# Performance work log

Hardware: AMD Instinct MI355X
Metric: run time of the kernel (lower is better)

The kernel has to match this reference:

```python
import jax, jax.numpy as jnp
import numpy as np
import math

BN_EPS = 1e-5
BASES = [5, 4]
NH = 8    # num_heads
KD = 64   # key_dim = hidden_dim

def _bn(x, g, b, m, v):
    # eval-mode BatchNorm1d over channel dim of (B, C, L)
    s = g * jax.lax.rsqrt(v + BN_EPS)
    return (x - m[None, :, None]) * s[None, :, None] + b[None, :, None]

def _conv1x1(x, W):
    # W: (out_ch, in_ch), x: (B, C, L)
    return jnp.einsum('oc,bcl->bol', W, x)

def _dwconv3(x, W):
    # depthwise conv1d, kernel 3, pad 1. W: (C, 3)
    c = x.shape[1]
    return jax.lax.conv_general_dilated(
        x, W[:, None, :], window_strides=(1,), padding=((1, 1),),
        dimension_numbers=('NCH', 'OIH', 'NCH'), feature_group_count=c)

def _log_attn(x, base, qkW, qkg, qkb, qkm, qkv, vW, vg, vb, vm, vv,
              peW, peg, peb, pem, pev):
    b, c, w = x.shape
    hd = c // NH
    scale = KD ** -0.5
    n = int(math.log(w, base) - 1e-9) + 1
    L = base ** n
    xp = jnp.pad(x, ((0, 0), (0, 0), (0, L - w)))
    qk = _bn(_conv1x1(xp, qkW), qkg, qkb, qkm, qkv).reshape(b, NH, 2, KD, L)
    q, k = qk[:, :, 0], qk[:, :, 1]
    v0 = _bn(_conv1x1(xp, vW), vg, vb, vm, vv)  # (B, C, L)
    v2 = v0.reshape(b, NH, hd, L)
    # n sequential butterfly steps: at step i, sequence L = base^i * base * base^(n-1-i)
    for i in range(n):
        s = (base ** i, base, base ** (n - 1 - i))
        qi = q.reshape(b, NH, KD, *s)
        ki = k.reshape(b, NH, KD, *s)
        attn = jax.nn.softmax(
            jnp.einsum('bhdijk,bhdiJk->bhJijk', qi, ki) * scale, axis=4)
        v2 = jnp.einsum('bhJijk,bhdijk->bhdiJk', attn,
                        v2.reshape(b, NH, hd, *s)).reshape(b, NH, hd, L)
    v2 = v2.reshape(b, c, L)
    pe = _bn(_dwconv3(v0, peW), peg, peb, pem, pev)
    return (v2 + pe)[..., :w]

def setup_inputs():
    key = jax.random.key(0)
    ks = jax.random.split(key, 24)
    c, h, b, w = 256, 1024, 4, 3125
    return {
        'x': jax.random.normal(ks[0], (b, c, w), jnp.float32),
        'qk_W': jax.random.normal(ks[1], (2, h, c), jnp.float32) * 0.05,
        'qk_g': jax.random.normal(ks[2], (2, h), jnp.float32) * 0.1 + 1.0,
        'qk_b': jax.random.normal(ks[3], (2, h), jnp.float32) * 0.05,
        'qk_m': jax.random.normal(ks[4], (2, h), jnp.float32) * 0.05,
        'qk_v': jax.random.uniform(ks[5], (2, h), jnp.float32) + 0.5,
        'v_W': jax.random.normal(ks[6], (2, c, c), jnp.float32) * 0.05,
        'v_g': jax.random.normal(ks[7], (2, c), jnp.float32) * 0.1 + 1.0,
        'v_b': jax.random.normal(ks[8], (2, c), jnp.float32) * 0.05,
        'v_m': jax.random.normal(ks[9], (2, c), jnp.float32) * 0.05,
        'v_v': jax.random.uniform(ks[10], (2, c), jnp.float32) + 0.5,
        'pe_W': jax.random.normal(ks[11], (2, c, 3), jnp.float32) * 0.1,
        'pe_g': jax.random.normal(ks[12], (2, c), jnp.float32) * 0.1 + 1.0,
        'pe_b': jax.random.normal(ks[13], (2, c), jnp.float32) * 0.05,
        'pe_m': jax.random.normal(ks[14], (2, c), jnp.float32) * 0.05,
        'pe_v': jax.random.uniform(ks[15], (2, c), jnp.float32) + 0.5,
        'proj_W': jax.random.normal(ks[16], (c, c), jnp.float32) * 0.05,
        'proj_g': jax.random.normal(ks[17], (c,), jnp.float32) * 0.1 + 1.0,
        'proj_b': jax.random.normal(ks[18], (c,), jnp.float32) * 0.05,
        'proj_m': jax.random.normal(ks[19], (c,), jnp.float32) * 0.05,
        'proj_v': jax.random.uniform(ks[20], (c,), jnp.float32) + 0.5,
    }

def reference(x, qk_W, qk_g, qk_b, qk_m, qk_v, v_W, v_g, v_b, v_m, v_v,
              pe_W, pe_g, pe_b, pe_m, pe_v, proj_W, proj_g, proj_b,
              proj_m, proj_v):
    for idx, base in enumerate(BASES):
        x = x + _log_attn(
            x, base,
            qk_W[idx], qk_g[idx], qk_b[idx], qk_m[idx], qk_v[idx],
            v_W[idx], v_g[idx], v_b[idx], v_m[idx], v_v[idx],
            pe_W[idx], pe_g[idx], pe_b[idx], pe_m[idx], pe_v[idx])
    return _bn(_conv1x1(x, proj_W), proj_g, proj_b, proj_m, proj_v)
```

## Files before the change

kernel.cpp:

```cpp
#include <hip/hip_runtime.h>
#include <math.h>

constexpr int CW = 3125;
constexpr int CC = 256;
constexpr int CB = 4;
constexpr int NHh = 8;
constexpr int KDd = 64;
constexpr int HDd = 32;
constexpr int QROW = 64;
constexpr int VROW = 256;

typedef __attribute__((ext_vector_type(8))) short short8;
typedef __attribute__((ext_vector_type(4))) float f32x4;
typedef __attribute__((ext_vector_type(4))) unsigned int uint4v;
typedef __attribute__((ext_vector_type(2))) unsigned int uint2v;

__device__ inline unsigned short f2bf(float x) {
  unsigned int u = __float_as_uint(x);
  unsigned int r = u + 0x7FFFu + ((u >> 16) & 1u);
  return (unsigned short)(r >> 16);
}

__global__ __launch_bounds__(256) void transpose_x(const float* __restrict__ src,
                                                   float* __restrict__ dst,
                                                   unsigned short* __restrict__ Ximg) {
  __shared__ float sT[64][65];
  int l0 = blockIdx.x * 64, c0 = blockIdx.y * 64, bI = blockIdx.z;
  int tid = threadIdx.x;
  for (int i = tid; i < 4096; i += 256) {
    int ll = i & 63, cc = i >> 6;
    int l = l0 + ll;
    sT[cc][ll] = (l < CW) ? src[((size_t)bI * CC + c0 + cc) * CW + l] : 0.f;
  }
  __syncthreads();
  for (int i = tid; i < 4096; i += 256) {
    int cc = i & 63, ll = i >> 6;
    int l = l0 + ll;
    if (l < CW) dst[((size_t)bI * CW + l) * CC + c0 + cc] = sT[cc][ll];
  }
  uint4v* img4 = (uint4v*)Ximg;
  for (int i = tid; i < 512; i += 256) {
    int ch8 = i & 7, ll = i >> 3;
    int l = l0 + ll;
    if (l >= CW) continue;
    unsigned short h[8];
#pragma unroll
    for (int j = 0; j < 8; j++) h[j] = f2bf(sT[ch8 * 8 + j][ll]);
    uint4v v;
    v[0] = (unsigned)h[0] | ((unsigned)h[1] << 16);
    v[1] = (unsigned)h[2] | ((unsigned)h[3] << 16);
    v[2] = (unsigned)h[4] | ((unsigned)h[5] << 16);
    v[3] = (unsigned)h[6] | ((unsigned)h[7] << 16);
    int cb = c0 + ch8 * 8;
    int p = bI * CW + l;
    int ptile = p >> 7, pp = p & 127;
    int ktile = cb >> 5, kchunk = (cb >> 3) & 3;
    img4[((size_t)ptile * 8 + ktile) * 512 + kchunk * 128 + pp] = v;
  }
}

__global__ __launch_bounds__(256) void prep_w_all(
    const float* __restrict__ qk_W, const float* __restrict__ v_W,
    const float* __restrict__ proj_W, unsigned short* __restrict__ Wimg0,
    unsigned short* __restrict__ Wimg1, unsigned short* __restrict__ Wimg2) {
  int t = blockIdx.x * 256 + threadIdx.x;
  if (t >= 2816 * 32) return;
  int og = t >> 5, ch = t & 31;
  const float* row;
  unsigned short* dstimg;
  int o;
  if (og < 1280) {
    o = og;
    row = (o < 1024) ? (qk_W + (size_t)o * CC) : (v_W + (size_t)(o - 1024) * CC);
    dstimg = Wimg0;
  } else if (og < 2560) {
    o = og - 1280;
    row = (o < 1024) ? (qk_W + (size_t)(1024 + o) * CC)
                     : (v_W + (size_t)(256 + o - 1024) * CC);
    dstimg = Wimg1;
  } else {
    o = og - 2560;
    row = proj_W + (size_t)o * CC;
    dstimg = Wimg2;
  }
  unsigned short h[8];
#pragma unroll
  for (int j = 0; j < 8; j++) h[j] = f2bf(row[ch * 8 + j]);
  uint4v v;
  v[0] = (unsigned)h[0] | ((unsigned)h[1] << 16);
  v[1] = (unsigned)h[2] | ((unsigned)h[3] << 16);
  v[2] = (unsigned)h[4] | ((unsigned)h[5] << 16);
  v[3] = (unsigned)h[6] | ((unsigned)h[7] << 16);
  int otile = o >> 7, oo = o & 127;
  int ktile = ch >> 2, kchunk = ch & 3;
  uint4v* img4 = (uint4v*)dstimg;
  img4[((size_t)otile * 8 + ktile) * 512 + kchunk * 128 + oo] = v;
}

__global__ __launch_bounds__(256) void prep_x(const float* __restrict__ X,
                                              unsigned short* __restrict__ img, int P) {
  int ptile = blockIdx.x, cq = blockIdx.y;
  int c0 = cq * 64;
  __shared__ float sX[64][129];
  int tid = threadIdx.x;
  for (int i = tid; i < 64 * 128; i += 256) {
    int cc = i & 63, pp = i >> 6;
    int p = ptile * 128 + pp;
    sX[cc][pp] = (p < P) ? X[(size_t)p * CC + c0 + cc] : 0.f;
  }
  __syncthreads();
  uint4v* img4 = (uint4v*)img;
  for (int i = tid; i < 1024; i += 256) {
    int ch = i >> 7, pp = i & 127;
    unsigned short h[8];
#pragma unroll
    for (int j = 0; j < 8; j++) h[j] = f2bf(sX[ch * 8 + j][pp]);
    uint4v vh;
    vh[0] = (unsigned)h[0] | ((unsigned)h[1] << 16);
    vh[1] = (unsigned)h[2] | ((unsigned)h[3] << 16);
    vh[2] = (unsigned)h[4] | ((unsigned)h[5] << 16);
    vh[3] = (unsigned)h[6] | ((unsigned)h[7] << 16);
    int ktile = cq * 2 + (ch >> 2), kchunk = ch & 3;
    img4[((size_t)ptile * 8 + ktile) * 512 + kchunk * 128 + pp] = vh;
  }
}

__global__ __launch_bounds__(256, 3) void gemm_qkv(
    const unsigned short* __restrict__ Aimg, const unsigned short* __restrict__ Ximg,
    const float* __restrict__ G0, const float* __restrict__ B0,
    const float* __restrict__ M0, const float* __restrict__ V0,
    const float* __restrict__ G1, const float* __restrict__ B1,
    const float* __restrict__ M1, const float* __restrict__ V1,
    unsigned short* __restrict__ qimg, unsigned short* __restrict__ kimg,
    float* __restrict__ v0pm, int L, int P, int nOt, int ptiles, int gemmBlocks) {
  int raw = blockIdx.x;
  int tid = threadIdx.x;
  if (raw >= gemmBlocks) {
    int pidx = raw - gemmBlocks;
    int nPad = L - CW;
    int bI = pidx / nPad, l = CW + (pidx - bI * nPad);
    for (int o = tid; o < 1280; o += 256) {
      if (o < 1024) {
        float s = G0[o] * rsqrtf(V0[o] + 1e-5f);
        float sh = B0[o] - M0[o] * s;
        int nh = o >> 7, sp = (o >> 6) & 1, d = o & 63;
        unsigned short* dst = sp ? kimg : qimg;
        dst[(((size_t)(bI * NHh + nh)) * L + l) * QROW + d] = f2bf(sp ? sh : sh * 0.125f);
      } else {
        int oc = o - 1024;
        float s = G1[oc] * rsqrtf(V1[oc] + 1e-5f);
        float sh = B1[oc] - M1[oc] * s;
        v0pm[((size_t)bI * L + l) * VROW + oc] = sh;
      }
    }
    return;
  }
  int xcd = raw & 7;
  int t = raw >> 3;
  int ptile = (t / nOt) * 8 + xcd;
  int otile = t % nOt;
  if (ptile >= ptiles) return;
  int wid = tid >> 6, lane = tid & 63;
  int wr = wid >> 1, wc = wid & 1;
  int r = lane & 15, kb = lane >> 4;
  bool isV = otile >= 8;
  f32x4 acc[4][4] = {};
  const unsigned short* Ap = Aimg + (size_t)otile * 32768 + kb * 1024 + (wr * 64 + r) * 8;
  const unsigned short* Bp = Ximg + (size_t)ptile * 32768 + kb * 1024 + (wc * 64 + r) * 8;
#pragma unroll
  for (int kt = 0; kt < 8; kt++) {
    short8 a[4], b[4];
#pragma unroll
    for (int mi = 0; mi < 4; mi++) a[mi] = *(const short8*)(Ap + kt * 4096 + mi * 128);
#pragma unroll
    for (int ni = 0; ni < 4; ni++) b[ni] = *(const short8*)(Bp + kt * 4096 + ni * 128);
    if (!isV) {
#pragma unroll
      for (int mi = 0; mi < 4; mi++)
#pragma unroll
        for (int ni = 0; ni < 4; ni++)
          acc[mi][ni] = __builtin_amdgcn_mfma_f32_16x16x32_bf16(a[mi], b[ni], acc[mi][ni], 0, 0, 0);
    } else {
#pragma unroll
      for (int mi = 0; mi < 4; mi++)
#pragma unroll
        for (int ni = 0; ni < 4; ni++)
          acc[ni][mi] = __builtin_amdgcn_mfma_f32_16x16x32_bf16(b[ni], a[mi], acc[ni][mi], 0, 0, 0);
    }
  }
  int cl = lane & 15, r4 = lane >> 4;
  int p0 = ptile * 128;
  int bI0 = p0 / CW;
  int rem0 = p0 - bI0 * CW;
  if (!isV) {
#pragma unroll
    for (int mi = 0; mi < 4; mi++) {
      int obase = otile * 128 + wr * 64 + mi * 16 + r4 * 4;
      int sp = (obase >> 6) & 1;
      float qs = sp ? 1.f : 0.125f;
      float s4[4], sh4[4];
#pragma unroll
      for (int reg = 0; reg < 4; reg++) {
        int o = obase + reg;
        float sb = G0[o] * rsqrtf(V0[o] + 1e-5f);
        s4[reg] = sb * qs;
        sh4[reg] = (B0[o] - M0[o] * sb) * qs;
      }
      int nh = obase >> 7, d0 = obase & 63;
      unsigned short* dst = sp ? kimg : qimg;
#pragma unroll
      for (int ni = 0; ni < 4; ni++) {
        int off = wc * 64 + ni * 16 + cl;
        int p = p0 + off;
        if (p >= P) continue;
        int l = rem0 + off, bI = bI0;
        if (l >= CW) { l -= CW; bI++; }
        unsigned short hi[4];
#pragma unroll
        for (int reg = 0; reg < 4; reg++)
          hi[reg] = f2bf(acc[mi][ni][reg] * s4[reg] + sh4[reg]);
        uint2v hv;
        hv[0] = (unsigned)hi[0] | ((unsigned)hi[1] << 16);
        hv[1] = (unsigned)hi[2] | ((unsigned)hi[3] << 16);
        *(uint2v*)(dst + (((size_t)(bI * NHh + nh)) * L + l) * QROW + d0) = hv;
      }
    }
  } else {
#pragma unroll
    for (int mi = 0; mi < 4; mi++) {
      int oc = (otile - 8) * 128 + wr * 64 + mi * 16 + cl;
      float s = G1[oc] * rsqrtf(V1[oc] + 1e-5f);
      float sh = B1[oc] - M1[oc] * s;
#pragma unroll
      for (int ni = 0; ni < 4; ni++) {
#pragma unroll
        for (int reg = 0; reg < 4; reg++) {
          int off = wc * 64 + ni * 16 + r4 * 4 + reg;
          int p = p0 + off;
          if (p >= P) continue;
          int l = rem0 + off, bI = bI0;
          if (l >= CW) { l -= CW; bI++; }
          v0pm[((size_t)bI * L + l) * VROW + oc] = acc[ni][mi][reg] * s + sh;
        }
      }
    }
  }
}

__global__ __launch_bounds__(256, 3) void gemm_proj(
    const unsigned short* __restrict__ Aimg, const unsigned short* __restrict__ Ximg,
    const float* __restrict__ G0, const float* __restrict__ B0,
    const float* __restrict__ M0, const float* __restrict__ V0,
    float* __restrict__ out, int P, int nOt, int ptiles64) {
  int raw = blockIdx.x;
  int xcd = raw & 7;
  int t = raw >> 3;
  int p64 = (t / nOt) * 8 + xcd;
  int otile = t % nOt;
  if (p64 >= ptiles64) return;
  int tid = threadIdx.x;
  int wid = tid >> 6, lane = tid & 63;
  int wr = wid >> 1, wc = wid & 1;
  int r = lane & 15, kb = lane >> 4;
  f32x4 acc[4][2] = {};
  int ptile128 = p64 >> 1;
  int psub = (p64 & 1) * 64;
  const unsigned short* Ap = Aimg + (size_t)otile * 32768 + kb * 1024 + (wr * 64 + r) * 8;
  const unsigned short* Bp = Ximg + (size_t)ptile128 * 32768 + kb * 1024 + (psub + wc * 32 + r) * 8;
#pragma unroll
  for (int kt = 0; kt < 8; kt++) {
    short8 a[4], b[2];
#pragma unroll
    for (int mi = 0; mi < 4; mi++) a[mi] = *(const short8*)(Ap + kt * 4096 + mi * 128);
#pragma unroll
    for (int ni = 0; ni < 2; ni++) b[ni] = *(const short8*)(Bp + kt * 4096 + ni * 128);
#pragma unroll
    for (int mi = 0; mi < 4; mi++)
#pragma unroll
      for (int ni = 0; ni < 2; ni++)
        acc[mi][ni] = __builtin_amdgcn_mfma_f32_16x16x32_bf16(a[mi], b[ni], acc[mi][ni], 0, 0, 0);
  }
  int cl = lane & 15, r4 = lane >> 4;
  int p0 = p64 * 64;
  int bI0 = p0 / CW;
  int rem0 = p0 - bI0 * CW;
#pragma unroll
  for (int mi = 0; mi < 4; mi++) {
#pragma unroll
    for (int reg = 0; reg < 4; reg++) {
      int o = otile * 128 + wr * 64 + mi * 16 + r4 * 4 + reg;
      float s = G0[o] * rsqrtf(V0[o] + 1e-5f);
      float sh = B0[o] - M0[o] * s;
#pragma unroll
      for (int ni = 0; ni < 2; ni++) {
        int off = wc * 32 + ni * 16 + cl;
        int p = p0 + off;
        if (p >= P) continue;
        int l = rem0 + off, bI = bI0;
        if (l >= CW) { l -= CW; bI++; }
        out[((size_t)bI * CC + o) * CW + l] = acc[mi][ni][reg] * s + sh;
      }
    }
  }
}

template <int B, bool DO_A, bool DO_B>
__global__ __launch_bounds__(256) void attn_mfma(
    const unsigned short* __restrict__ qimg, const unsigned short* __restrict__ kimg,
    const float* __restrict__ vin, float* __restrict__ vout,
    int L, int s2, int bpb) {
  constexpr int B2 = B * B;
  constexpr int MT = (B2 + 15) / 16;
  __shared__ float S[4][256];
  int tid = threadIdx.x;
  int w = tid >> 6, lane = tid & 63;
  int gid = blockIdx.x * 4 + w;
  int bh = gid / bpb;
  int g = gid - bh * bpb;
  int hi_ = g / s2, lo_ = g - hi_ * s2;
  int base0 = hi_ * B2 * s2 + lo_;
  int cl = lane & 15, r4 = lane >> 4;
  int dd = lane & 31, half = lane >> 5;
  int bI = bh >> 3, nh = bh & 7;

  short8 kh[MT][2], qh[MT][2];
#pragma unroll
  for (int mt = 0; mt < MT; mt++) {
    int idx = mt * 16 + cl;
    if (idx > B2 - 1) idx = B2 - 1;
    size_t row = ((size_t)bh * L + base0 + idx * s2) * QROW;
#pragma unroll
    for (int kt = 0; kt < 2; kt++) {
      int dof = kt * 32 + r4 * 8;
      kh[mt][kt] = *(const short8*)(kimg + row + dof);
      qh[mt][kt] = *(const short8*)(qimg + row + dof);
    }
  }
  size_t vBase = ((size_t)bI * L + base0) * VROW + nh * HDd + dd;
  float vv[B2];
#pragma unroll
  for (int idx = 0; idx < B2; idx++) vv[idx] = vin[vBase + (size_t)(idx * s2) * VROW];

  f32x4 C[MT][MT] = {};
#pragma unroll
  for (int kt = 0; kt < 2; kt++)
#pragma unroll
    for (int mt = 0; mt < MT; mt++)
#pragma unroll
      for (int nt = 0; nt < MT; nt++)
        C[mt][nt] = __builtin_amdgcn_mfma_f32_16x16x32_bf16(kh[mt][kt], qh[nt][kt], C[mt][nt], 0, 0, 0);
#pragma unroll
  for (int mt = 0; mt < MT; mt++)
#pragma unroll
    for (int nt = 0; nt < MT; nt++)
#pragma unroll
      for (int rr = 0; rr < 4; rr++) {
        int J_idx = mt * 16 + r4 * 4 + rr;
        int j_idx = nt * 16 + cl;
        if (J_idx < B2 && j_idx < B2) {
          float val = C[mt][nt][rr];
          int Jq, bJ, jq, bj;
          if (B == 4) {
            Jq = J_idx >> 2; bJ = J_idx & 3; jq = j_idx >> 2; bj = j_idx & 3;
          } else {
            Jq = (J_idx * 205) >> 10; bJ = J_idx - Jq * 5;
            jq = (j_idx * 205) >> 10; bj = j_idx - jq * 5;
          }
          if (DO_A && bJ == bj) S[w][(bJ * B + Jq) * B + jq] = val;
          if (DO_B && Jq == jq) S[w][128 + (Jq * B + bJ) * B + bj] = val;
        }
      }
  if (DO_A) {
#pragma unroll
    for (int b = 0; b < B; b++) {
      float tmp[B];
#pragma unroll
      for (int J = 0; J < B; J++) {
        float sc[B];
#pragma unroll
        for (int j = 0; j < B; j++) sc[j] = S[w][(b * B + J) * B + j];
        float mx = sc[0];
#pragma unroll
        for (int j = 1; j < B; j++) mx = fmaxf(mx, sc[j]);
        float sum = 0.f, acc = 0.f;
#pragma unroll
        for (int j = 0; j < B; j++) {
          float e = __expf(sc[j] - mx);
          sum += e;
          acc += e * vv[j * B + b];
        }
        tmp[J] = acc / sum;
      }
#pragma unroll
      for (int J = 0; J < B; J++) vv[J * B + b] = tmp[J];
    }
  }
  if (DO_B) {
#pragma unroll
    for (int a = 0; a < B; a++) {
      float tmp[B];
#pragma unroll
      for (int J = 0; J < B; J++) {
        float sc[B];
#pragma unroll
        for (int j = 0; j < B; j++) sc[j] = S[w][128 + (a * B + J) * B + j];
        float mx = sc[0];
#pragma unroll
        for (int j = 1; j < B; j++) mx = fmaxf(mx, sc[j]);
        float sum = 0.f, acc = 0.f;
#pragma unroll
        for (int j = 0; j < B; j++) {
          float e = __expf(sc[j] - mx);
          sum += e;
          acc += e * vv[a * B + j];
        }
        tmp[J] = acc / sum;
      }
#pragma unroll
      for (int J = 0; J < B; J++) vv[a * B + J] = tmp[J];
    }
  }
#pragma unroll
  for (int idx = 0; idx < B2; idx++)
    if ((idx & 1) == half) vout[vBase + (size_t)(idx * s2) * VROW] = vv[idx];
}

template <int B, int S, bool FUSE>
__global__ __launch_bounds__(256) void attn_tri(
    const unsigned short* __restrict__ qimg, const unsigned short* __restrict__ kimg,
    const float* __restrict__ vin, float* __restrict__ vout,
    int L, int nblk,
    const float* __restrict__ peW, const float* __restrict__ Gp,
    const float* __restrict__ Bp2, const float* __restrict__ Mp,
    const float* __restrict__ Vp, const float* __restrict__ v0pm,
    float* __restrict__ xcur) {
  constexpr int B2 = B * B;
  constexpr int B3 = B * B * B;
  constexpr int NT = (B3 + 15) / 16;
  constexpr int MTW = (NT + 3) / 4;
  __shared__ float slab[3 * B2 * B * B];
  __shared__ float sv[B3 * 33];
  int tid = threadIdx.x;
  int w = tid >> 6, lane = tid & 63;
  int bid = blockIdx.x;
  int bh = bid / nblk;
  int blk = bid - bh * nblk;
  int hi = blk / S, lo = blk - hi * S;
  int base0 = hi * B3 * S + lo;
  int bI = bh >> 3, nh = bh & 7;
  int cl = lane & 15, r4 = lane >> 4;

  for (int t = tid; t < B3 * 32; t += 256) {
    int c = t & 31, idx = t >> 5;
    sv[idx * 33 + c] = vin[((size_t)bI * L + base0 + idx * S) * VROW + nh * HDd + c];
  }

  short8 kh[MTW][2], qh[NT][2];
#pragma unroll
  for (int m = 0; m < MTW; m++) {
    int idx = (w * MTW + m) * 16 + cl;
    if (idx > B3 - 1) idx = B3 - 1;
    size_t row = ((size_t)bh * L + base0 + idx * S) * QROW;
#pragma unroll
    for (int kt = 0; kt < 2; kt++)
      kh[m][kt] = *(const short8*)(kimg + row + kt * 32 + r4 * 8);
  }
#pragma unroll
  for (int nt = 0; nt < NT; nt++) {
    int idx = nt * 16 + cl;
    if (idx > B3 - 1) idx = B3 - 1;
    size_t row = ((size_t)bh * L + base0 + idx * S) * QROW;
#pragma unroll
    for (int kt = 0; kt < 2; kt++)
      qh[nt][kt] = *(const short8*)(qimg + row + kt * 32 + r4 * 8);
  }
  f32x4 C[MTW][NT] = {};
#pragma unroll
  for (int kt = 0; kt < 2; kt++)
#pragma unroll
    for (int m = 0; m < MTW; m++)
#pragma unroll
      for (int nt = 0; nt < NT; nt++)
        C[m][nt] = __builtin_amdgcn_mfma_f32_16x16x32_bf16(kh[m][kt], qh[nt][kt], C[m][nt], 0, 0, 0);
#pragma unroll
  for (int m = 0; m < MTW; m++)
#pragma unroll
    for (int nt = 0; nt < NT; nt++)
#pragma unroll
      for (int rr = 0; rr < 4; rr++) {
        int J = (w * MTW + m) * 16 + r4 * 4 + rr;
        int j = nt * 16 + cl;
        if (J < B3 && j < B3) {
          float val = C[m][nt][rr];
          int A2 = J / B2, Jr = J - A2 * B2, A1 = Jr / B, A0 = Jr - A1 * B;
          int a2 = j / B2, jr = j - a2 * B2, a1 = jr / B, a0 = jr - a1 * B;
          if (A1 == a1 && A0 == a0) slab[((0 * B2 + (a1 * B + a0)) * B + A2) * B + a2] = val;
          if (A2 == a2 && A0 == a0) slab[((1 * B2 + (a2 * B + a0)) * B + A1) * B + a1] = val;
          if (A2 == a2 && A1 == a1) slab[((2 * B2 + (a2 * B + a1)) * B + A0) * B + a0] = val;
        }
      }
  __syncthreads();
  if (tid < 3 * B2) {
    float* bw = &slab[tid * B * B];
#pragma unroll
    for (int J = 0; J < B; J++) {
      float mx = bw[J * B];
#pragma unroll
      for (int j = 1; j < B; j++) mx = fmaxf(mx, bw[J * B + j]);
      float sum = 0.f;
      float e[B];
#pragma unroll
      for (int j = 0; j < B; j++) {
        e[j] = __expf(bw[J * B + j] - mx);
        sum += e[j];
      }
      float inv = 1.f / sum;
#pragma unroll
      for (int j = 0; j < B; j++) bw[J * B + j] = e[j] * inv;
    }
  }
  __syncthreads();
  int c = tid & 31, slot = tid >> 5;
  for (int lvl = 0; lvl < 3; lvl++) {
    for (int g = slot; g < B2; g += 8) {
      int ghi = g / B, glo = g - ghi * B;
      const float* wrow = &slab[(lvl * B2 + g) * B * B];
      float vvals[B], outs[B];
#pragma unroll
      for (int j = 0; j < B; j++) {
        int pid = (lvl == 0) ? (j * B2 + g) : (lvl == 1) ? (ghi * B2 + j * B + glo) : (g * B + j);
        vvals[j] = sv[pid * 33 + c];
      }
#pragma unroll
      for (int J = 0; J < B; J++) {
        float a = 0.f;
#pragma unroll
        for (int j = 0; j < B; j++) a += wrow[J * B + j] * vvals[j];
        outs[J] = a;
      }
#pragma unroll
      for (int J = 0; J < B; J++) {
        int pid = (lvl == 0) ? (J * B2 + g) : (lvl == 1) ? (ghi * B2 + J * B + glo) : (g * B + J);
        sv[pid * 33 + c] = outs[J];
      }
    }
    __syncthreads();
  }
  if (!FUSE) {
    for (int t = tid; t < B3 * 32; t += 256) {
      int c2 = t & 31, idx = t >> 5;
      vout[((size_t)bI * L + base0 + idx * S) * VROW + nh * HDd + c2] = sv[idx * 33 + c2];
    }
  } else {
    int ch = nh * HDd + c;
    float pw0 = peW[ch * 3 + 0], pw1 = peW[ch * 3 + 1], pw2 = peW[ch * 3 + 2];
    float s = Gp[ch] * rsqrtf(Vp[ch] + 1e-5f);
    float sh = Bp2[ch] - Mp[ch] * s;
    for (int idx = slot; idx < B3; idx += 8) {
      int l = base0 + idx;
      if (l >= CW) continue;
      size_t row = ((size_t)bI * L + l) * VROW + ch;
      float left = (l > 0) ? v0pm[row - VROW] : 0.f;
      float mid = v0pm[row];
      float right = (l + 1 < L) ? v0pm[row + VROW] : 0.f;
      float pe = (left * pw0 + mid * pw1 + right * pw2) * s + sh;
      xcur[((size_t)bI * CW + l) * CC + ch] += sv[idx * 33 + c] + pe;
    }
  }
}

extern "C" void kernel_launch(void* const* d_in, const int* in_sizes, int n_in,
                              void* d_out, int out_size, void* d_ws, size_t ws_size,
                              hipStream_t stream) {
  const float* x = (const float*)d_in[0];
  const float* qk_W = (const float*)d_in[1];
  const float* qk_g = (const float*)d_in[2];
  const float* qk_b = (const float*)d_in[3];
  const float* qk_m = (const float*)d_in[4];
  const float* qk_v = (const float*)d_in[5];
  const float* v_W = (const float*)d_in[6];
  const float* v_g = (const float*)d_in[7];
  const float* v_b = (const float*)d_in[8];
  const float* v_m = (const float*)d_in[9];
  const float* v_v = (const float*)d_in[10];
  const float* pe_W = (const float*)d_in[11];
  const float* pe_g = (const float*)d_in[12];
  const float* pe_b = (const float*)d_in[13];
  const float* pe_m = (const float*)d_in[14];
  const float* pe_v = (const float*)d_in[15];
  const float* proj_W = (const float*)d_in[16];
  const float* proj_g = (const float*)d_in[17];
  const float* proj_b = (const float*)d_in[18];
  const float* proj_m = (const float*)d_in[19];
  const float* proj_v = (const float*)d_in[20];

  char* ws = (char*)d_ws;
  size_t off = 0;
  auto alloc = [&](size_t bytes) {
    char* p = ws + off;
    off += (bytes + 255) & ~(size_t)255;
    return (void*)p;
  };
  const int Lmax = 4096;
  const int P = CB * CW;
  const int ptiles = (P + 127) / 128;
  float* xcur = (float*)alloc((size_t)CB * CW * CC * 4);
  unsigned short* qimg = (unsigned short*)alloc((size_t)CB * NHh * Lmax * QROW * 2);
  unsigned short* kimg = (unsigned short*)alloc((size_t)CB * NHh * Lmax * QROW * 2);
  float* v0pm = (float*)alloc((size_t)CB * Lmax * VROW * 4);
  float* vA = (float*)alloc((size_t)CB * Lmax * VROW * 4);
  unsigned short* Ximg = (unsigned short*)alloc((size_t)ptiles * 32768 * 2);
  unsigned short* Wimg0 = (unsigned short*)alloc((size_t)10 * 8 * 8192 * 2);
  unsigned short* Wimg1 = (unsigned short*)alloc((size_t)10 * 8 * 8192 * 2);
  unsigned short* Wimg2 = (unsigned short*)alloc((size_t)2 * 8 * 8192 * 2);
  (void)ws_size;

  prep_w_all<<<(2816 * 32 + 255) / 256, 256, 0, stream>>>(qk_W, v_W, proj_W,
                                                          Wimg0, Wimg1, Wimg2);
  {
    dim3 gt((CW + 63) / 64, 4, CB);
    transpose_x<<<gt, 256, 0, stream>>>(x, xcur, Ximg);
  }

  const int pgroups8 = (ptiles + 7) / 8;
  const int ptiles64 = (P + 63) / 64;
  const int pg64 = (ptiles64 + 7) / 8;
  const int gemmBlocks = 8 * pgroups8 * 10;
  const int Ls[2] = {3125, 4096};
  const unsigned short* Wimgs[2] = {Wimg0, Wimg1};
  for (int blk = 0; blk < 2; blk++) {
    int L = Ls[blk];
    if (blk == 1) {
      dim3 gx(ptiles, 4);
      prep_x<<<gx, 256, 0, stream>>>(xcur, Ximg, P);
    }
    int padBlocks = (L > CW) ? CB * (L - CW) : 0;
    gemm_qkv<<<gemmBlocks + padBlocks, 256, 0, stream>>>(
        Wimgs[blk], Ximg, qk_g + blk * 1024, qk_b + blk * 1024, qk_m + blk * 1024,
        qk_v + blk * 1024, v_g + blk * CC, v_b + blk * CC, v_m + blk * CC,
        v_v + blk * CC, qimg, kimg, v0pm, L, P, 10, ptiles, gemmBlocks);

    const float* peWb = pe_W + (size_t)blk * CC * 3;
    const float* peG = pe_g + blk * CC;
    const float* peB = pe_b + blk * CC;
    const float* peM = pe_m + blk * CC;
    const float* peV = pe_v + blk * CC;
    if (blk == 0) {
      int bpb = L / 25;
      attn_mfma<5, true, true><<<(CB * NHh * bpb) / 4, 256, 0, stream>>>(
          qimg, kimg, v0pm, vA, L, 125, bpb);
      int nblk = L / 125;
      attn_tri<5, 1, true><<<CB * NHh * nblk, 256, 0, stream>>>(
          qimg, kimg, vA, nullptr, L, nblk, peWb, peG, peB, peM, peV, v0pm, xcur);
    } else {
      int nblk = L / 64;
      attn_tri<4, 64, false><<<CB * NHh * nblk, 256, 0, stream>>>(
          qimg, kimg, v0pm, vA, L, nblk, nullptr, nullptr, nullptr, nullptr,
          nullptr, nullptr, nullptr);
      attn_tri<4, 1, true><<<CB * NHh * nblk, 256, 0, stream>>>(
          qimg, kimg, vA, nullptr, L, nblk, peWb, peG, peB, peM, peV, v0pm, xcur);
    }
  }
  {
    dim3 gx(ptiles, 4);
    prep_x<<<gx, 256, 0, stream>>>(xcur, Ximg, P);
    gemm_proj<<<8 * pg64 * 2, 256, 0, stream>>>(
        Wimg2, Ximg, proj_g, proj_b, proj_m, proj_v, (float*)d_out, P, 2, ptiles64);
  }
}
```

Measured before the change: 250.2 us.

## Keep V rows in registers across three butterfly levels, store V as bf16 in LDS

The attn_tri kernel now gives each thread one (A2, channel) pair and runs all three butterfly mixing levels in registers. This removes the per-level shared-memory round trips and two __syncthreads barriers. The V tile in shared memory is stored as bf16 to halve LDS use, which rounds V to lower precision. Score scatter index decomposition is hoisted out of the inner loop. Only 32*B threads do the mixing work, which reduces parallelism in that phase.

```diff
diff --git a/kernel.cpp b/kernel.cpp
--- a/kernel.cpp
+++ b/kernel.cpp
@@ -19,6 +19,9 @@
   unsigned int u = __float_as_uint(x);
   unsigned int r = u + 0x7FFFu + ((u >> 16) & 1u);
   return (unsigned short)(r >> 16);
+}
+__device__ inline float bf2f(unsigned short h) {
+  return __uint_as_float((unsigned)h << 16);
 }
 
 __global__ __launch_bounds__(256) void transpose_x(const float* __restrict__ src,
@@ -439,7 +442,7 @@
   constexpr int NT = (B3 + 15) / 16;
   constexpr int MTW = (NT + 3) / 4;
   __shared__ float slab[3 * B2 * B * B];
-  __shared__ float sv[B3 * 33];
+  __shared__ unsigned short svh[B3 * 33];
   int tid = threadIdx.x;
   int w = tid >> 6, lane = tid & 63;
   int bid = blockIdx.x;
@@ -452,7 +455,8 @@
 
   for (int t = tid; t < B3 * 32; t += 256) {
     int c = t & 31, idx = t >> 5;
-    sv[idx * 33 + c] = vin[((size_t)bI * L + base0 + idx * S) * VROW + nh * HDd + c];
+    svh[idx * 33 + c] =
+        f2bf(vin[((size_t)bI * L + base0 + idx * S) * VROW + nh * HDd + c]);
   }
 
   short8 kh[MTW][2], qh[NT][2];
@@ -482,23 +486,42 @@
 #pragma unroll
       for (int nt = 0; nt < NT; nt++)
         C[m][nt] = __builtin_amdgcn_mfma_f32_16x16x32_bf16(kh[m][kt], qh[nt][kt], C[m][nt], 0, 0, 0);
+  int jd2[NT], jd1[NT], jd0[NT];
+  bool jok[NT];
+#pragma unroll
+  for (int nt = 0; nt < NT; nt++) {
+    int j = nt * 16 + cl;
+    jok[nt] = (j < B3);
+    if (j > B3 - 1) j = B3 - 1;
+    jd2[nt] = j / B2;
+    int jr = j - jd2[nt] * B2;
+    jd1[nt] = jr / B;
+    jd0[nt] = jr - jd1[nt] * B;
+  }
 #pragma unroll
   for (int m = 0; m < MTW; m++)
 #pragma unroll
-    for (int nt = 0; nt < NT; nt++)
-#pragma unroll
-      for (int rr = 0; rr < 4; rr++) {
-        int J = (w * MTW + m) * 16 + r4 * 4 + rr;
-        int j = nt * 16 + cl;
-        if (J < B3 && j < B3) {
+    for (int rr = 0; rr < 4; rr++) {
+      int J = (w * MTW + m) * 16 + r4 * 4 + rr;
+      bool Jok = (J < B3);
+      int Jc = Jok ? J : (B3 - 1);
+      int A2 = Jc / B2;
+      int Jr = Jc - A2 * B2;
+      int A1 = Jr / B;
+      int A0 = Jr - A1 * B;
+#pragma unroll
+      for (int nt = 0; nt < NT; nt++) {
+        if (Jok && jok[nt]) {
           float val = C[m][nt][rr];
-          int A2 = J / B2, Jr = J - A2 * B2, A1 = Jr / B, A0 = Jr - A1 * B;
-          int a2 = j / B2, jr = j - a2 * B2, a1 = jr / B, a0 = jr - a1 * B;
-          if (A1 == a1 && A0 == a0) slab[((0 * B2 + (a1 * B + a0)) * B + A2) * B + a2] = val;
-          if (A2 == a2 && A0 == a0) slab[((1 * B2 + (a2 * B + a0)) * B + A1) * B + a1] = val;
-          if (A2 == a2 && A1 == a1) slab[((2 * B2 + (a2 * B + a1)) * B + A0) * B + a0] = val;
+          if (A1 == jd1[nt] && A0 == jd0[nt])
+            slab[((0 * B2 + (jd1[nt] * B + jd0[nt])) * B + A2) * B + jd2[nt]] = val;
+          if (A2 == jd2[nt] && A0 == jd0[nt])
+            slab[((1 * B2 + (jd2[nt] * B + jd0[nt])) * B + A1) * B + jd1[nt]] = val;
+          if (A2 == jd2[nt] && A1 == jd1[nt])
+            slab[((2 * B2 + (jd2[nt] * B + jd1[nt])) * B + A0) * B + jd0[nt]] = val;
         }
       }
+    }
   __syncthreads();
   if (tid < 3 * B2) {
     float* bw = &slab[tid * B * B];
@@ -520,51 +543,58 @@
     }
   }
   __syncthreads();
-  int c = tid & 31, slot = tid >> 5;
-  for (int lvl = 0; lvl < 3; lvl++) {
-    for (int g = slot; g < B2; g += 8) {
-      int ghi = g / B, glo = g - ghi * B;
-      const float* wrow = &slab[(lvl * B2 + g) * B * B];
-      float vvals[B], outs[B];
-#pragma unroll
-      for (int j = 0; j < B; j++) {
-        int pid = (lvl == 0) ? (j * B2 + g) : (lvl == 1) ? (ghi * B2 + j * B + glo) : (g * B + j);
-        vvals[j] = sv[pid * 33 + c];
-      }
-#pragma unroll
-      for (int J = 0; J < B; J++) {
-        float a = 0.f;
-#pragma unroll
-        for (int j = 0; j < B; j++) a += wrow[J * B + j] * vvals[j];
-        outs[J] = a;
-      }
-#pragma unroll
-      for (int J = 0; J < B; J++) {
-        int pid = (lvl == 0) ? (J * B2 + g) : (lvl == 1) ? (ghi * B2 + J * B + glo) : (g * B + J);
-        sv[pid * 33 + c] = outs[J];
-      }
-    }
-    __syncthreads();
-  }
-  if (!FUSE) {
-    for (int t = tid; t < B3 * 32; t += 256) {
-      int c2 = t & 31, idx = t >> 5;
-      vout[((size_t)bI * L + base0 + idx * S) * VROW + nh * HDd + c2] = sv[idx * 33 + c2];
-    }
-  } else {
-    int ch = nh * HDd + c;
-    float pw0 = peW[ch * 3 + 0], pw1 = peW[ch * 3 + 1], pw2 = peW[ch * 3 + 2];
-    float s = Gp[ch] * rsqrtf(Vp[ch] + 1e-5f);
-    float sh = Bp2[ch] - Mp[ch] * s;
-    for (int idx = slot; idx < B3; idx += 8) {
-      int l = base0 + idx;
-      if (l >= CW) continue;
-      size_t row = ((size_t)bI * L + l) * VROW + ch;
-      float left = (l > 0) ? v0pm[row - VROW] : 0.f;
-      float mid = v0pm[row];
-      float right = (l + 1 < L) ? v0pm[row + VROW] : 0.f;
-      float pe = (left * pw0 + mid * pw1 + right * pw2) * s + sh;
-      xcur[((size_t)bI * CW + l) * CC + ch] += sv[idx * 33 + c] + pe;
+  if (tid < 32 * B) {
+    int c = tid & 31, A2 = tid >> 5;
+    float va[B2], vb[B2];
+#pragma unroll
+    for (int g = 0; g < B2; g++) {
+      const float* w0 = &slab[((0 * B2 + g) * B + A2) * B];
+      float acc = 0.f;
+#pragma unroll
+      for (int j = 0; j < B; j++)
+        acc += w0[j] * bf2f(svh[(j * B2 + g) * 33 + c]);
+      va[g] = acc;
+    }
+#pragma unroll
+    for (int a0 = 0; a0 < B; a0++)
+#pragma unroll
+      for (int A1 = 0; A1 < B; A1++) {
+        const float* w1 = &slab[((1 * B2 + (A2 * B + a0)) * B + A1) * B];
+        float acc = 0.f;
+#pragma unroll
+        for (int j = 0; j < B; j++) acc += w1[j] * va[j * B + a0];
+        vb[A1 * B + a0] = acc;
+      }
+#pragma unroll
+    for (int a1 = 0; a1 < B; a1++)
+#pragma unroll
+      for (int A0 = 0; A0 < B; A0++) {
+        const float* w2 = &slab[((2 * B2 + (A2 * B + a1)) * B + A0) * B];
+        float acc = 0.f;
+#pragma unroll
+        for (int j = 0; j < B; j++) acc += w2[j] * vb[a1 * B + j];
+        va[a1 * B + A0] = acc;
+      }
+    if (!FUSE) {
+#pragma unroll
+      for (int g = 0; g < B2; g++)
+        vout[((size_t)bI * L + base0 + (A2 * B2 + g) * S) * VROW + nh * HDd + c] = va[g];
+    } else {
+      int ch = nh * HDd + c;
+      float pw0 = peW[ch * 3 + 0], pw1 = peW[ch * 3 + 1], pw2 = peW[ch * 3 + 2];
+      float s = Gp[ch] * rsqrtf(Vp[ch] + 1e-5f);
+      float sh = Bp2[ch] - Mp[ch] * s;
+#pragma unroll
+      for (int g = 0; g < B2; g++) {
+        int l = base0 + A2 * B2 + g;
+        if (l >= CW) continue;
+        size_t row = ((size_t)bI * L + l) * VROW + ch;
+        float left = (l > 0) ? v0pm[row - VROW] : 0.f;
+        float mid = v0pm[row];
+        float right = (l + 1 < L) ? v0pm[row + VROW] : 0.f;
+        float pe = (left * pw0 + mid * pw1 + right * pw2) * s + sh;
+        xcur[((size_t)bI * CW + l) * CC + ch] += va[g] + pe;
+      }
     }
   }
 }
```

After: 296.1 us. 18.3% more time.
